# Kernel optimization log

Measured on AMD Instinct MI355X. Metric: run time of the kernel, lower is better.

The kernel has to match this reference:

```python
import jax, jax.numpy as jnp
import numpy as np

N_NODES = 50000
N_EDGES = 800000
IN_CH = 128
HID = 64
OUT_CH = 64


def sage_conv(x, src, dst, w_l, w_r, b, num_nodes):
    """PyG SAGEConv with mean aggregation: lin_l(mean_j x_j) + lin_r(x_i)."""
    # gather source features and scatter-mean into destination nodes
    agg = jax.ops.segment_sum(x[src], dst, num_segments=num_nodes)          # [N, C]
    deg = jax.ops.segment_sum(jnp.ones((src.shape[0],), x.dtype), dst,
                              num_segments=num_nodes)                        # [N]
    mean = agg / jnp.maximum(deg, 1.0)[:, None]
    return mean @ w_l + x @ w_r + b


def setup_inputs() -> dict:
    key = jax.random.key(0)
    k = jax.random.split(key, 8)
    x = jax.random.normal(k[0], (N_NODES, IN_CH), dtype=jnp.float32)
    edge_index = jax.random.randint(k[1], (2, N_EDGES), 0, N_NODES, dtype=jnp.int32)
    s1 = 1.0 / np.sqrt(IN_CH)
    s2 = 1.0 / np.sqrt(HID)
    w1_l = jax.random.uniform(k[2], (IN_CH, HID), jnp.float32, -s1, s1)
    w1_r = jax.random.uniform(k[3], (IN_CH, HID), jnp.float32, -s1, s1)
    b1 = jax.random.uniform(k[4], (HID,), jnp.float32, -s1, s1)
    w2_l = jax.random.uniform(k[5], (HID, OUT_CH), jnp.float32, -s2, s2)
    w2_r = jax.random.uniform(k[6], (HID, OUT_CH), jnp.float32, -s2, s2)
    b2 = jax.random.uniform(k[7], (OUT_CH,), jnp.float32, -s2, s2)
    return {"x": x, "edge_index": edge_index,
            "w1_l": w1_l, "w1_r": w1_r, "b1": b1,
            "w2_l": w2_l, "w2_r": w2_r, "b2": b2}


def reference(x, edge_index, w1_l, w1_r, b1, w2_l, w2_r, b2):
    src, dst = edge_index[0], edge_index[1]
    num_nodes = x.shape[0]
    h = jax.nn.relu(sage_conv(x, src, dst, w1_l, w1_r, b1, num_nodes))
    out = jax.nn.relu(sage_conv(h, src, dst, w2_l, w2_r, b2, num_nodes))
    return out
```

## Files before the change

### kernel.cpp

```cpp
#include <hip/hip_runtime.h>
#include <hip/hip_fp16.h>

#define DEGCAP 64
#define NB_MAX 256
#define BCAP 5120
#define TILE 4000

typedef _Float16 half8 __attribute__((ext_vector_type(8)));
typedef float float4v __attribute__((ext_vector_type(4)));

__global__ __launch_bounds__(256) void prep(int* __restrict__ bCursor,
                                            const float* __restrict__ w1l,
                                            const float* __restrict__ w1r,
                                            const float* __restrict__ w2l,
                                            const float* __restrict__ w2r,
                                            _Float16* __restrict__ Wt1,
                                            _Float16* __restrict__ Wt2) {
    const int gtid = blockIdx.x * 256 + threadIdx.x;
    const int gstride = gridDim.x * 256;
    if (gtid < NB_MAX) bCursor[gtid] = 0;
    for (int i = gtid; i < 128 * 128; i += gstride) {
        int c = i >> 7, k = i & 127;
        const float* W = (c < 64) ? w1l : w1r;
        Wt1[c * 128 + k] = (_Float16)W[k * 64 + (c & 63)];
    }
    for (int i = gtid; i < 128 * 64; i += gstride) {
        int c = i >> 6, k = i & 63;
        const float* W = (c < 64) ? w2l : w2r;
        Wt2[c * 64 + k] = (_Float16)W[k * 64 + (c & 63)];
    }
}

template <int K, bool AF32>
__device__ __forceinline__ void gemm_body(const void* __restrict__ Av,
                                          const _Float16* __restrict__ Wt,
                                          unsigned short* __restrict__ Clh,
                                          unsigned short* __restrict__ Trh,
                                          int M, int blk) {
    constexpr int NS = K / 32;
    const int tid = threadIdx.x;
    const int row0 = blk * 64;
    const int wv = tid >> 6;
    const int lane = tid & 63;
    const int qd = lane >> 4;
    const int lr = lane & 15;
    const int col = wv * 16 + lr;

    half8 bl[NS], br[NS];
    #pragma unroll
    for (int s = 0; s < NS; ++s) {
        bl[s] = *(const half8*)&Wt[col * K + s * 32 + qd * 8];
        br[s] = *(const half8*)&Wt[(64 + col) * K + s * 32 + qd * 8];
    }

    half8 a[4][NS];
    #pragma unroll
    for (int i = 0; i < 4; ++i) {
        const int gr = row0 + i * 16 + lr;
        const bool ok = gr < M;
        if constexpr (AF32) {
            const float* Arow = (const float*)Av + (long long)gr * K;
            #pragma unroll
            for (int s = 0; s < NS; ++s) {
                float4 t0 = make_float4(0.f, 0.f, 0.f, 0.f);
                float4 t1 = make_float4(0.f, 0.f, 0.f, 0.f);
                if (ok) {
                    t0 = *(const float4*)&Arow[s * 32 + qd * 8];
                    t1 = *(const float4*)&Arow[s * 32 + qd * 8 + 4];
                }
                half8 h;
                h[0] = (_Float16)t0.x; h[1] = (_Float16)t0.y;
                h[2] = (_Float16)t0.z; h[3] = (_Float16)t0.w;
                h[4] = (_Float16)t1.x; h[5] = (_Float16)t1.y;
                h[6] = (_Float16)t1.z; h[7] = (_Float16)t1.w;
                a[i][s] = h;
            }
        } else {
            const _Float16* Arow = (const _Float16*)Av + (long long)gr * K;
            #pragma unroll
            for (int s = 0; s < NS; ++s) {
                a[i][s] = ok ? *(const half8*)&Arow[s * 32 + qd * 8]
                             : (half8){0, 0, 0, 0, 0, 0, 0, 0};
            }
        }
    }

    float4v accL[4], accR[4];
    #pragma unroll
    for (int i = 0; i < 4; ++i) {
        accL[i] = (float4v){0.f, 0.f, 0.f, 0.f};
        accR[i] = (float4v){0.f, 0.f, 0.f, 0.f};
    }

    #pragma unroll
    for (int i = 0; i < 4; ++i) {
        #pragma unroll
        for (int s = 0; s < NS; ++s) {
            accL[i] = __builtin_amdgcn_mfma_f32_16x16x32_f16(a[i][s], bl[s], accL[i], 0, 0, 0);
            accR[i] = __builtin_amdgcn_mfma_f32_16x16x32_f16(a[i][s], br[s], accR[i], 0, 0, 0);
        }
    }

    #pragma unroll
    for (int i = 0; i < 4; ++i) {
        #pragma unroll
        for (int rg = 0; rg < 4; ++rg) {
            int gr = row0 + i * 16 + qd * 4 + rg;
            if (gr < M) {
                Clh[(long long)gr * 64 + col] = __half_as_ushort(__float2half_rn(accL[i][rg]));
                Trh[(long long)gr * 64 + col] = __half_as_ushort(__float2half_rn(accR[i][rg]));
            }
        }
    }
}

__global__ __launch_bounds__(256) void fused_scatter_gemm1(
        const int* __restrict__ src, const int* __restrict__ dst,
        int* __restrict__ bCursor, unsigned int* __restrict__ gPacked,
        int E, int NB, int scatterBlocks,
        const float* __restrict__ A, const _Float16* __restrict__ Wt1,
        unsigned short* __restrict__ Clh, unsigned short* __restrict__ Trh,
        int M) {
    __shared__ __align__(16) char smem[22048];
    const int tid = threadIdx.x;

    if ((int)blockIdx.x < scatterBlocks) {
        unsigned int* spv = (unsigned int*)smem;
        unsigned char* sbuk = (unsigned char*)(smem + 16000);
        int* hist = (int*)(smem + 20000);
        int* cur  = (int*)(smem + 21024);

        const int t0 = blockIdx.x * TILE;
        const int len = (E - t0) < TILE ? (E - t0) : TILE;

        hist[tid] = 0;
        __syncthreads();
        for (int j = tid; j < len; j += 256) {
            int d = dst[t0 + j];
            int s = src[t0 + j];
            int b = d >> 8;
            sbuk[j] = (unsigned char)b;
            spv[j] = ((unsigned int)(d & 255) << 17) | (unsigned int)s;
            atomicAdd(&hist[b], 1);
        }
        __syncthreads();
        if (tid < NB && hist[tid] > 0)
            cur[tid] = tid * BCAP + atomicAdd(&bCursor[tid], hist[tid]);
        __syncthreads();
        for (int j = tid; j < len; j += 256) {
            int b = sbuk[j];
            int pos = atomicAdd(&cur[b], 1);
            if (pos < (b + 1) * BCAP) gPacked[pos] = spv[j];
        }
    } else {
        gemm_body<128, true>(A, Wt1, Clh, Trh, M, (int)blockIdx.x - scatterBlocks);
    }
}

__global__ __launch_bounds__(256) void bucket_build(const unsigned int* __restrict__ gPacked,
                                                    const int* __restrict__ bCursor,
                                                    int* __restrict__ deg,
                                                    unsigned short* __restrict__ ssrc,
                                                    int N) {
    __shared__ int cnt[256];
    const int tid = threadIdx.x;
    const int b = blockIdx.x;
    const int base = b * BCAP;
    int C = bCursor[b];
    if (C > BCAP) C = BCAP;

    cnt[tid] = 0;
    __syncthreads();
    for (int j = tid; j < C; j += 256) {
        unsigned int v = gPacked[base + j];
        int ln = v >> 17;
        int pos = atomicAdd(&cnt[ln], 1);
        if (pos < DEGCAP)
            ssrc[(long long)(b * 256 + ln) * DEGCAP + pos] = (unsigned short)(v & 0x1FFFFu);
    }
    __syncthreads();
    int node = b * 256 + tid;
    if (node < N) deg[node] = cnt[tid] < DEGCAP ? cnt[tid] : DEGCAP;
}

__global__ __launch_bounds__(256) void gemm2(const _Float16* __restrict__ Ah,
                                             const _Float16* __restrict__ Wt2,
                                             unsigned short* __restrict__ Clh,
                                             unsigned short* __restrict__ Trh,
                                             int M) {
    gemm_body<64, false>(Ah, Wt2, Clh, Trh, M, (int)blockIdx.x);
}

template <bool OUTH>
__global__ __launch_bounds__(256) void agg_combine(const unsigned int* __restrict__ tl2,
                                                   const unsigned int* __restrict__ trh2,
                                                   const float* __restrict__ bias,
                                                   const int* __restrict__ deg_,
                                                   const unsigned short* __restrict__ ssrc,
                                                   void* __restrict__ outv, int N) {
    int w = (blockIdx.x * 256 + threadIdx.x) >> 6;
    int lane = threadIdx.x & 63;
    if (w >= N) return;
    int deg = deg_[w];
    int n = deg < DEGCAP ? deg : DEGCAP;
    int g2 = lane >> 4;
    int c8 = lane & 15;

    int sid = (lane < n) ? (int)ssrc[(long long)w * DEGCAP + lane] : 0;

    float ax0 = 0.f, ay0 = 0.f, ax1 = 0.f, ay1 = 0.f;

    #pragma unroll 2
    for (int jj = 0; jj < n; jj += 8) {
        int e0 = __shfl(sid, jj + g2, 64);
        int e1 = __shfl(sid, jj + 4 + g2, 64);
        bool v0 = (jj + g2) < n;
        bool v1 = (jj + 4 + g2) < n;
        uint2 u0 = make_uint2(0u, 0u), u1 = make_uint2(0u, 0u);
        if (v0) u0 = *(const uint2*)&tl2[(long long)e0 * 32 + c8 * 2];
        if (v1) u1 = *(const uint2*)&tl2[(long long)e1 * 32 + c8 * 2];
        float2 f;
        f = __half22float2(*(__half2*)&u0.x); ax0 += f.x; ay0 += f.y;
        f = __half22float2(*(__half2*)&u0.y); ax1 += f.x; ay1 += f.y;
        f = __half22float2(*(__half2*)&u1.x); ax0 += f.x; ay0 += f.y;
        f = __half22float2(*(__half2*)&u1.y); ax1 += f.x; ay1 += f.y;
    }

    ax0 += __shfl_xor(ax0, 16, 64);
    ay0 += __shfl_xor(ay0, 16, 64);
    ax1 += __shfl_xor(ax1, 16, 64);
    ay1 += __shfl_xor(ay1, 16, 64);
    ax0 += __shfl_xor(ax0, 32, 64);
    ay0 += __shfl_xor(ay0, 32, 64);
    ax1 += __shfl_xor(ax1, 32, 64);
    ay1 += __shfl_xor(ay1, 32, 64);

    if (g2 == 0) {
        float d = (float)(deg > 1 ? deg : 1);
        uint2 tu = *(const uint2*)&trh2[(long long)w * 32 + c8 * 2];
        float2 t0 = __half22float2(*(__half2*)&tu.x);
        float2 t1 = __half22float2(*(__half2*)&tu.y);
        float4 bb = *(const float4*)&bias[c8 * 4];
        float v0 = fmaxf(ax0 / d + t0.x + bb.x, 0.f);
        float v1 = fmaxf(ay0 / d + t0.y + bb.y, 0.f);
        float v2 = fmaxf(ax1 / d + t1.x + bb.z, 0.f);
        float v3 = fmaxf(ay1 / d + t1.y + bb.w, 0.f);
        if (OUTH) {
            __half2 h0 = __floats2half2_rn(v0, v1);
            __half2 h1 = __floats2half2_rn(v2, v3);
            uint2 st;
            st.x = *(unsigned int*)&h0;
            st.y = *(unsigned int*)&h1;
            ((uint2*)outv)[(long long)w * 16 + c8] = st;
        } else {
            ((float4*)outv)[(long long)w * 16 + c8] = make_float4(v0, v1, v2, v3);
        }
    }
}

extern "C" void kernel_launch(void* const* d_in, const int* in_sizes, int n_in,
                              void* d_out, int out_size, void* d_ws, size_t ws_size,
                              hipStream_t stream) {
    const float* x   = (const float*)d_in[0];
    const int*   ei  = (const int*)d_in[1];
    const float* w1l = (const float*)d_in[2];
    const float* w1r = (const float*)d_in[3];
    const float* b1  = (const float*)d_in[4];
    const float* w2l = (const float*)d_in[5];
    const float* w2r = (const float*)d_in[6];
    const float* b2  = (const float*)d_in[7];
    float* out = (float*)d_out;

    const int N = in_sizes[0] / 128;
    const int E = in_sizes[1] / 2;
    const int* src = ei;
    const int* dst = ei + E;
    const int NB = (N + 255) >> 8;

    auto alignup = [](size_t v) { return (v + 255) & ~(size_t)255; };
    char* p = (char*)d_ws;
    int* bCursor = (int*)p;                    p += alignup(NB_MAX * sizeof(int));
    int* deg     = (int*)p;                    p += alignup((size_t)N * sizeof(int));
    unsigned int* gPacked = (unsigned int*)p;  p += alignup((size_t)NB_MAX * BCAP * sizeof(unsigned int));
    unsigned short* ssrc = (unsigned short*)p; p += alignup((size_t)N * DEGCAP * sizeof(unsigned short));
    const long long NC = (long long)N * 64;
    unsigned short* tlh = (unsigned short*)p;  p += alignup((size_t)NC * sizeof(unsigned short));
    unsigned short* trh = (unsigned short*)p;  p += alignup((size_t)NC * sizeof(unsigned short));
    unsigned short* hh  = (unsigned short*)p;  p += alignup((size_t)NC * sizeof(unsigned short));
    _Float16* Wt1 = (_Float16*)p;              p += alignup(128 * 128 * sizeof(_Float16));
    _Float16* Wt2 = (_Float16*)p;              p += alignup(128 * 64 * sizeof(_Float16));

    const int scatterBlocks = (E + TILE - 1) / TILE;
    const int gemmBlocks = (N + 63) / 64;
    const int aggBlocks = (int)((NC + 255) / 256);

    prep<<<96, 256, 0, stream>>>(bCursor, w1l, w1r, w2l, w2r, Wt1, Wt2);

    fused_scatter_gemm1<<<scatterBlocks + gemmBlocks, 256, 0, stream>>>(
        src, dst, bCursor, gPacked, E, NB, scatterBlocks,
        x, Wt1, tlh, trh, N);

    bucket_build<<<NB, 256, 0, stream>>>(gPacked, bCursor, deg, ssrc, N);

    agg_combine<true><<<aggBlocks, 256, 0, stream>>>((const unsigned int*)tlh,
                                                     (const unsigned int*)trh,
                                                     b1, deg, ssrc, hh, N);

    gemm2<<<gemmBlocks, 256, 0, stream>>>((const _Float16*)hh, Wt2, tlh, trh, N);
    agg_combine<false><<<aggBlocks, 256, 0, stream>>>((const unsigned int*)tlh,
                                                      (const unsigned int*)trh,
                                                      b2, deg, ssrc, out, N);
}
```

Measured before the change: 179.9 us.

## Aggregate four nodes per wavefront with 16-lane groups instead of one node per wave

The aggregation kernel changes from one 64-lane wavefront per destination node, which needed a cross-lane reduction, to 16-lane groups that each own one node. Each group loads its neighbour index list as packed uint2 values and walks it four edges at a time, so the xor-shuffle reduction goes away and fewer lanes sit idle when degree is small. The cost is less memory-level parallelism per node: neighbours are processed serially within the group, and loads are issued even for padded slots past the node's degree. Those extra loads use stale but in-bounds indices, and their results are discarded.

```diff
diff --git a/kernel.cpp b/kernel.cpp
--- a/kernel.cpp
+++ b/kernel.cpp
@@ -192,68 +192,74 @@
 }
 
 template <bool OUTH>
-__global__ __launch_bounds__(256) void agg_combine(const unsigned int* __restrict__ tl2,
-                                                   const unsigned int* __restrict__ trh2,
-                                                   const float* __restrict__ bias,
-                                                   const int* __restrict__ deg_,
-                                                   const unsigned short* __restrict__ ssrc,
-                                                   void* __restrict__ outv, int N) {
-    int w = (blockIdx.x * 256 + threadIdx.x) >> 6;
-    int lane = threadIdx.x & 63;
-    if (w >= N) return;
-    int deg = deg_[w];
-    int n = deg < DEGCAP ? deg : DEGCAP;
-    int g2 = lane >> 4;
-    int c8 = lane & 15;
-
-    int sid = (lane < n) ? (int)ssrc[(long long)w * DEGCAP + lane] : 0;
-
-    float ax0 = 0.f, ay0 = 0.f, ax1 = 0.f, ay1 = 0.f;
-
-    #pragma unroll 2
-    for (int jj = 0; jj < n; jj += 8) {
-        int e0 = __shfl(sid, jj + g2, 64);
-        int e1 = __shfl(sid, jj + 4 + g2, 64);
-        bool v0 = (jj + g2) < n;
-        bool v1 = (jj + 4 + g2) < n;
-        uint2 u0 = make_uint2(0u, 0u), u1 = make_uint2(0u, 0u);
-        if (v0) u0 = *(const uint2*)&tl2[(long long)e0 * 32 + c8 * 2];
-        if (v1) u1 = *(const uint2*)&tl2[(long long)e1 * 32 + c8 * 2];
+__global__ __launch_bounds__(256) void agg_group(const uint2* __restrict__ TL,
+                                                 const uint2* __restrict__ TR,
+                                                 const float* __restrict__ bias,
+                                                 const int* __restrict__ deg_,
+                                                 const uint2* __restrict__ ssrc2,
+                                                 void* __restrict__ outv, int N) {
+    const int tid = threadIdx.x;
+    const int wv = tid >> 6;
+    const int lane = tid & 63;
+    const int c = lane & 15;
+    const int w = (int)blockIdx.x * 16 + wv * 4 + (lane >> 4);
+    const bool ok = w < N;
+
+    const int deg = ok ? deg_[w] : 0;
+    const int n = deg < DEGCAP ? deg : DEGCAP;
+
+    uint2 su = ok ? ssrc2[(size_t)w * 16 + c] : make_uint2(0u, 0u);
+
+    float a0 = 0.f, a1 = 0.f, a2 = 0.f, a3 = 0.f;
+
+    for (int j = 0; j < n; j += 4) {
+        const int b = (lane & 48) + (j >> 2);
+        unsigned sx = __shfl((int)su.x, b, 64);
+        unsigned sy = __shfl((int)su.y, b, 64);
+        int e0 = (int)(sx & 0xFFFFu);
+        int e1 = (int)(sx >> 16);
+        int e2 = (int)(sy & 0xFFFFu);
+        int e3 = (int)(sy >> 16);
+        uint2 q0 = TL[e0 * 16 + c];
+        uint2 q1 = TL[e1 * 16 + c];
+        uint2 q2 = TL[e2 * 16 + c];
+        uint2 q3 = TL[e3 * 16 + c];
         float2 f;
-        f = __half22float2(*(__half2*)&u0.x); ax0 += f.x; ay0 += f.y;
-        f = __half22float2(*(__half2*)&u0.y); ax1 += f.x; ay1 += f.y;
-        f = __half22float2(*(__half2*)&u1.x); ax0 += f.x; ay0 += f.y;
-        f = __half22float2(*(__half2*)&u1.y); ax1 += f.x; ay1 += f.y;
-    }
-
-    ax0 += __shfl_xor(ax0, 16, 64);
-    ay0 += __shfl_xor(ay0, 16, 64);
-    ax1 += __shfl_xor(ax1, 16, 64);
-    ay1 += __shfl_xor(ay1, 16, 64);
-    ax0 += __shfl_xor(ax0, 32, 64);
-    ay0 += __shfl_xor(ay0, 32, 64);
-    ax1 += __shfl_xor(ax1, 32, 64);
-    ay1 += __shfl_xor(ay1, 32, 64);
-
-    if (g2 == 0) {
+        f = __half22float2(*(__half2*)&q0.x); a0 += f.x; a1 += f.y;
+        f = __half22float2(*(__half2*)&q0.y); a2 += f.x; a3 += f.y;
+        if (j + 1 < n) {
+            f = __half22float2(*(__half2*)&q1.x); a0 += f.x; a1 += f.y;
+            f = __half22float2(*(__half2*)&q1.y); a2 += f.x; a3 += f.y;
+        }
+        if (j + 2 < n) {
+            f = __half22float2(*(__half2*)&q2.x); a0 += f.x; a1 += f.y;
+            f = __half22float2(*(__half2*)&q2.y); a2 += f.x; a3 += f.y;
+        }
+        if (j + 3 < n) {
+            f = __half22float2(*(__half2*)&q3.x); a0 += f.x; a1 += f.y;
+            f = __half22float2(*(__half2*)&q3.y); a2 += f.x; a3 += f.y;
+        }
+    }
+
+    if (ok) {
         float d = (float)(deg > 1 ? deg : 1);
-        uint2 tu = *(const uint2*)&trh2[(long long)w * 32 + c8 * 2];
+        uint2 tu = TR[(size_t)w * 16 + c];
         float2 t0 = __half22float2(*(__half2*)&tu.x);
         float2 t1 = __half22float2(*(__half2*)&tu.y);
-        float4 bb = *(const float4*)&bias[c8 * 4];
-        float v0 = fmaxf(ax0 / d + t0.x + bb.x, 0.f);
-        float v1 = fmaxf(ay0 / d + t0.y + bb.y, 0.f);
-        float v2 = fmaxf(ax1 / d + t1.x + bb.z, 0.f);
-        float v3 = fmaxf(ay1 / d + t1.y + bb.w, 0.f);
+        float4 bb = *(const float4*)&bias[c * 4];
+        float v0 = fmaxf(a0 / d + t0.x + bb.x, 0.f);
+        float v1 = fmaxf(a1 / d + t0.y + bb.y, 0.f);
+        float v2 = fmaxf(a2 / d + t1.x + bb.z, 0.f);
+        float v3 = fmaxf(a3 / d + t1.y + bb.w, 0.f);
         if (OUTH) {
             __half2 h0 = __floats2half2_rn(v0, v1);
             __half2 h1 = __floats2half2_rn(v2, v3);
             uint2 st;
             st.x = *(unsigned int*)&h0;
             st.y = *(unsigned int*)&h1;
-            ((uint2*)outv)[(long long)w * 16 + c8] = st;
+            ((uint2*)outv)[(size_t)w * 16 + c] = st;
         } else {
-            ((float4*)outv)[(long long)w * 16 + c8] = make_float4(v0, v1, v2, v3);
+            ((float4*)outv)[(size_t)w * 16 + c] = make_float4(v0, v1, v2, v3);
         }
     }
 }
@@ -292,7 +298,7 @@
 
     const int scatterBlocks = (E + TILE - 1) / TILE;
     const int gemmBlocks = (N + 63) / 64;
-    const int aggBlocks = (int)((NC + 255) / 256);
+    const int aggBlocks = (N + 15) / 16;
 
     prep<<<96, 256, 0, stream>>>(bCursor, w1l, w1r, w2l, w2r, Wt1, Wt2);
 
@@ -302,12 +308,15 @@
 
     bucket_build<<<NB, 256, 0, stream>>>(gPacked, bCursor, deg, ssrc, N);
 
-    agg_combine<true><<<aggBlocks, 256, 0, stream>>>((const unsigned int*)tlh,
-                                                     (const unsigned int*)trh,
-                                                     b1, deg, ssrc, hh, N);
+    agg_group<true><<<aggBlocks, 256, 0, stream>>>((const uint2*)tlh,
+                                                   (const uint2*)trh,
+                                                   b1, deg, (const uint2*)ssrc,
+                                                   hh, N);
 
     gemm2<<<gemmBlocks, 256, 0, stream>>>((const _Float16*)hh, Wt2, tlh, trh, N);
-    agg_combine<false><<<aggBlocks, 256, 0, stream>>>((const unsigned int*)tlh,
-                                                      (const unsigned int*)trh,
-                                                      b2, deg, ssrc, out, N);
-}
+
+    agg_group<false><<<aggBlocks, 256, 0, stream>>>((const uint2*)tlh,
+                                                    (const uint2*)trh,
+                                                    b2, deg, (const uint2*)ssrc,
+                                                    out, N);
+}
```

Result: faster. 172.1 us (-4.3%).
